# Performance work log

Measured on AMD Instinct MI355X. Metric: run time of the kernel, lower is better.

## Reference

```python
import jax, jax.numpy as jnp
import numpy as np
import math

B, S, HID = 2, 2048, 1024
NH = 16
HD = HID // NH


def setup_inputs() -> dict:
    key = jax.random.key(0)
    ks = jax.random.split(key, 5)
    std = 1.0 / math.sqrt(HID)
    return {
        "x": jax.random.normal(ks[0], (B, S, HID), dtype=jnp.float32),
        "wq": jax.random.normal(ks[1], (HID, HID), dtype=jnp.float32) * std,
        "wk": jax.random.normal(ks[2], (HID, HID), dtype=jnp.float32) * std,
        "wv": jax.random.normal(ks[3], (HID, HID), dtype=jnp.float32) * std,
        "wo": jax.random.normal(ks[4], (HID, HID), dtype=jnp.float32) * std,
    }


def reference(x, wq, wk, wv, wo):
    # x: [B, S, HID]; weights stored as nn.Linear weight [out, in] -> y = x @ W.T
    b, s, _ = x.shape
    scale = 1.0 / math.sqrt(HD)

    def heads(t):  # [B, S, HID] -> [B, NH, S, HD]
        return t.reshape(b, s, NH, HD).transpose(0, 2, 1, 3)

    q = heads(x @ wq.T)
    k = heads(x @ wk.T)
    v = heads(x @ wv.T)

    # single ring step (cp_size=1): streaming-LSE causal attention
    scores = jnp.einsum("bhqd,bhkd->bhqk", q, k) * scale  # [B, NH, S, S]
    q_idx = jnp.arange(s)[:, None]
    k_idx = jnp.arange(s)[None, :]
    causal_mask = k_idx > q_idx  # [S, S]
    scores = jnp.where(causal_mask, -jnp.inf, scores)

    local_max = jnp.max(scores, axis=-1, keepdims=True)
    exp_scores = jnp.exp(scores - local_max)
    local_sum = jnp.sum(exp_scores, axis=-1, keepdims=True)
    attn_num = jnp.einsum("bhqk,bhkd->bhqd", exp_scores, v)
    attn_out = attn_num / (local_sum + 1e-8)  # [B, NH, S, HD]

    attn_out = attn_out.transpose(0, 2, 1, 3).reshape(b, s, HID)
    return attn_out @ wo.T
```

## Files before the change

kernel.cpp:

```cpp
#include <hip/hip_runtime.h>
#include <hip/hip_bf16.h>

#define S_LEN 2048
#define NHEAD 16
#define HDIM 64
#define HID 1024
#define BATCH 2
#define TSTR 136

typedef __attribute__((ext_vector_type(8))) short s16x8;
typedef __attribute__((ext_vector_type(4))) short s16x4;
typedef __attribute__((ext_vector_type(4))) float f32x4;

__device__ __forceinline__ short f2bf(float f) {
    union { __hip_bfloat16 b; short s; } u;
    u.b = __float2bfloat16(f);
    return u.s;
}
__device__ __forceinline__ float fexp2(float x) {
    return __builtin_amdgcn_exp2f(x);
}
__device__ __forceinline__ f32x4 mfma16(s16x8 a, s16x8 b, f32x4 c) {
    return __builtin_amdgcn_mfma_f32_16x16x32_bf16(a, b, c, 0, 0, 0);
}
__device__ __forceinline__ void gload16(const short* g, short* l) {
    __builtin_amdgcn_global_load_lds(
        (const __attribute__((address_space(1))) void*)g,
        (__attribute__((address_space(3))) void*)l, 16, 0, 0);
}
__device__ __forceinline__ unsigned bfpack(float a, float b) {
    unsigned ua = __builtin_bit_cast(unsigned, a) + 0x8000u;
    unsigned ub = __builtin_bit_cast(unsigned, b) + 0x8000u;
    return (ub & 0xFFFF0000u) | (ua >> 16);
}

__global__ __launch_bounds__(256) void convert_kernel(
    const float* __restrict__ x,  const float* __restrict__ wq,
    const float* __restrict__ wk, const float* __restrict__ wv,
    const float* __restrict__ wo,
    short* __restrict__ xb, short* __restrict__ wcat, short* __restrict__ wob)
{
    const int F4X = 1048576, F4W = 262144;
    const int total = F4X + 4 * F4W;
    for (int i = blockIdx.x * blockDim.x + threadIdx.x; i < total;
         i += gridDim.x * blockDim.x) {
        const float4* s; short* d; int off;
        if (i < F4X)              { s = (const float4*)x;  d = xb;             off = i; }
        else if (i < F4X + F4W)   { s = (const float4*)wq; d = wcat;           off = i - F4X; }
        else if (i < F4X + 2*F4W) { s = (const float4*)wk; d = wcat + 1048576; off = i - (F4X + F4W); }
        else if (i < F4X + 3*F4W) { s = (const float4*)wv; d = wcat + 2097152; off = i - (F4X + 2*F4W); }
        else                      { s = (const float4*)wo; d = wob;            off = i - (F4X + 3*F4W); }
        float4 v = s[off];
        s16x4 o4 = { f2bf(v.x), f2bf(v.y), f2bf(v.z), f2bf(v.w) };
        *(s16x4*)(d + (size_t)off * 4) = o4;
    }
}

__global__ __launch_bounds__(256) void qkv_gemm2(
    const short* __restrict__ xb, const short* __restrict__ wcat,
    short* __restrict__ q_ws, short* __restrict__ k_ws, short* __restrict__ vt_ws)
{
    __shared__ union SM {
        struct { short A[128][64]; short B[128][64]; } s;
        short T[128][TSTR];
    } sm;
    const int t = threadIdx.x;
    const int lane = t & 63, w = t >> 6;
    const int g = lane >> 4, r15 = lane & 15;
    const int wm = w >> 1, wn = w & 1;
    const int bid = blockIdx.x;
    const int cx = bid & 7, ii = bid >> 3;
    const int mt = cx * 4 + (ii & 3), nt = ii >> 2;
    const int m0 = mt * 128, n0 = nt * 128;
    const int sel = n0 >> 10;
    const int nr0 = n0 & 1023;
    const short* Ag = (sel == 2) ? (wcat + (size_t)(2048 + nr0) * 1024)
                                 : (xb   + (size_t)m0 * 1024);
    const short* Bg = (sel == 2) ? (xb   + (size_t)m0 * 1024)
                                 : (wcat + (size_t)(sel * 1024 + nr0) * 1024);
    const int lrow = lane >> 3;
    const int scol = ((lane & 7) ^ lrow) * 8;
    const int rsw = r15 & 7;

    f32x4 acc[4][4] = {};

    for (int k0 = 0; k0 < 1024; k0 += 64) {
        __syncthreads();
        #pragma unroll
        for (int ch = 0; ch < 4; ++ch) {
            const int row = w * 32 + ch * 8;
            gload16(Ag + (size_t)(row + lrow) * 1024 + k0 + scol, &sm.s.A[row][0]);
            gload16(Bg + (size_t)(row + lrow) * 1024 + k0 + scol, &sm.s.B[row][0]);
        }
        __syncthreads();
        #pragma unroll
        for (int kk = 0; kk < 2; ++kk) {
            s16x8 af[4], bfr[4];
            #pragma unroll
            for (int mi = 0; mi < 4; ++mi)
                af[mi] = *(const s16x8*)&sm.s.A[wm * 64 + mi * 16 + r15][((kk * 4 + g) ^ rsw) * 8];
            #pragma unroll
            for (int ni = 0; ni < 4; ++ni)
                bfr[ni] = *(const s16x8*)&sm.s.B[wn * 64 + ni * 16 + r15][((kk * 4 + g) ^ rsw) * 8];
            #pragma unroll
            for (int mi = 0; mi < 4; ++mi)
                #pragma unroll
                for (int ni = 0; ni < 4; ++ni)
                    acc[mi][ni] = mfma16(af[mi], bfr[ni], acc[mi][ni]);
        }
    }

    __syncthreads();
    #pragma unroll
    for (int mi = 0; mi < 4; ++mi)
    #pragma unroll
    for (int ni = 0; ni < 4; ++ni)
        #pragma unroll
        for (int reg = 0; reg < 4; ++reg)
            sm.T[wm * 64 + mi * 16 + g * 4 + reg][wn * 64 + ni * 16 + r15]
                = f2bf(acc[mi][ni][reg]);
    __syncthreads();

    const int b = m0 >> 11;
    const int ms = m0 & 2047;
    #pragma unroll
    for (int it = 0; it < 8; ++it) {
        int u = w + it * 4;
        int half = u & 1;
        int rg = u >> 1;
        int r = rg * 8 + lrow;
        int colc = half * 64 + (lane & 7) * 8;
        s16x8 v = *(const s16x8*)&sm.T[r][colc];
        if (sel == 2) {
            int n = nr0 + r;
            int h = n >> 6, d = n & 63;
            *(s16x8*)(vt_ws + ((size_t)(b * NHEAD + h) * HDIM + d) * S_LEN + ms + colc) = v;
        } else {
            int s = ms + r;
            int n = nr0 + colc;
            int h = n >> 6, d = n & 63;
            short* dst = (sel == 0) ? q_ws : k_ws;
            *(s16x8*)(dst + ((size_t)(b * NHEAD + h) * S_LEN + s) * HDIM + d) = v;
        }
    }
}

__global__ __launch_bounds__(256) void attn_kernel2(
    const short* __restrict__ q_ws, const short* __restrict__ k_ws,
    const short* __restrict__ vt_ws, short* __restrict__ attn_ws)
{
    __shared__ short Ks[2][64][64];
    __shared__ short Vts[2][64][64];
    const int t = threadIdx.x;
    const int lane = t & 63, w = t >> 6;
    const int g = lane >> 4, r15 = lane & 15;
    const int bid = blockIdx.x;
    const int lb = (bid & 7) * 64 + (bid >> 3);
    const int p = lb & 15;
    const int bh = lb >> 4;
    const size_t base = (size_t)bh * S_LEN * HDIM;
    const float KSC = 0.18033688f;
    const int swr = (r15 & 7) << 3;
    const int r0 = t >> 3, c0 = (t & 7) * 8;
    const int cx0 = c0 ^ ((r0 & 7) << 3);
    const int b = bh >> 4, h = bh & 15;
    const int qloc = w * 16 + r15;

    union P8 { unsigned u[4]; s16x8 v; };
    union V8 { s16x4 h[2]; s16x8 v; };

    for (int phase = 0; phase < 2; ++phase) {
        const int qt = phase ? (31 - p) : p;
        const int q0 = qt * 64;
        const int ntk = qt + 1;
        const int qg = q0 + qloc;
        s16x8 qf0 = *(const s16x8*)(q_ws + base + (size_t)qg * HDIM + g * 8);
        s16x8 qf1 = *(const s16x8*)(q_ws + base + (size_t)qg * HDIM + 32 + g * 8);
        f32x4 o[4] = {};
        float mrun = -1e30f, lrun_p = 0.f;

        *(s16x8*)&Ks[0][r0][cx0]        = *(const s16x8*)(k_ws  + base + (size_t)r0 * HDIM + c0);
        *(s16x8*)&Ks[0][r0 + 32][cx0]   = *(const s16x8*)(k_ws  + base + (size_t)(r0 + 32) * HDIM + c0);
        *(s16x8*)&Vts[0][r0][cx0]       = *(const s16x8*)(vt_ws + base + (size_t)r0 * S_LEN + c0);
        *(s16x8*)&Vts[0][r0 + 32][cx0]  = *(const s16x8*)(vt_ws + base + (size_t)(r0 + 32) * S_LEN + c0);
        __syncthreads();

        const short* kpa = k_ws  + base + (size_t)(64 + r0) * HDIM + c0;
        const short* kpb = kpa + 32 * HDIM;
        const short* vpa = vt_ws + base + (size_t)r0 * S_LEN + 64 + c0;
        const short* vpb = vpa + 32 * S_LEN;

        for (int kt = 0; kt < ntk; ++kt) {
            const int cur = kt & 1;
            const bool pre = (kt + 1 < ntk);
            const bool dg = (kt == ntk - 1);
            s16x8 ka, kb, va, vb;
            if (pre) {
                ka = *(const s16x8*)kpa;  kb = *(const s16x8*)kpb;
                va = *(const s16x8*)vpa;  vb = *(const s16x8*)vpb;
                kpa += 64 * HDIM; kpb += 64 * HDIM; vpa += 64; vpb += 64;
            }

            s16x8 kfa[4][2];
            #pragma unroll
            for (int f = 0; f < 4; ++f)
                #pragma unroll
                for (int c = 0; c < 2; ++c)
                    kfa[f][c] = *(const s16x8*)&Ks[cur][f * 16 + r15][(c * 32 + g * 8) ^ swr];
            V8 vfr[4][2];
            #pragma unroll
            for (int f2 = 0; f2 < 4; ++f2)
                #pragma unroll
                for (int kc = 0; kc < 2; ++kc) {
                    vfr[f2][kc].h[0] = *(const s16x4*)&Vts[cur][f2 * 16 + r15][(kc * 32 + g * 4) ^ swr];
                    vfr[f2][kc].h[1] = *(const s16x4*)&Vts[cur][f2 * 16 + r15][(kc * 32 + 16 + g * 4) ^ swr];
                }

            f32x4 z[4];
            __builtin_amdgcn_s_setprio(1);
            #pragma unroll
            for (int f = 0; f < 4; ++f) {
                f32x4 zz = { 0.f, 0.f, 0.f, 0.f };
                zz = mfma16(kfa[f][0], qf0, zz);
                zz = mfma16(kfa[f][1], qf1, zz);
                z[f] = zz;
            }
            __builtin_amdgcn_s_setprio(0);

            if (dg) {
                #pragma unroll
                for (int f = 0; f < 4; ++f)
                    #pragma unroll
                    for (int reg = 0; reg < 4; ++reg)
                        if (f * 16 + g * 4 + reg > qloc) z[f][reg] = -3e30f;
            }

            float zf[4];
            #pragma unroll
            for (int f = 0; f < 4; ++f)
                zf[f] = fmaxf(fmaxf(z[f][0], z[f][1]), fmaxf(z[f][2], z[f][3]));
            float zm = fmaxf(fmaxf(zf[0], zf[1]), fmaxf(zf[2], zf[3]));
            zm = fmaxf(zm, __shfl_xor(zm, 16));
            zm = fmaxf(zm, __shfl_xor(zm, 32));
            float pm = zm * KSC;

            if (!__all(pm - mrun <= 8.0f)) {
                float newm = fmaxf(mrun, pm);
                float sc = fexp2(mrun - newm);
                #pragma unroll
                for (int f2 = 0; f2 < 4; ++f2) o[f2] *= sc;
                lrun_p *= sc;
                mrun = newm;
            }

            P8 p8[2];
            #pragma unroll
            for (int f = 0; f < 4; ++f) {
                float e0 = fexp2(__builtin_fmaf(z[f][0], KSC, -mrun));
                float e1 = fexp2(__builtin_fmaf(z[f][1], KSC, -mrun));
                float e2 = fexp2(__builtin_fmaf(z[f][2], KSC, -mrun));
                float e3 = fexp2(__builtin_fmaf(z[f][3], KSC, -mrun));
                lrun_p += (e0 + e1) + (e2 + e3);
                p8[f >> 1].u[(f & 1) * 2]     = bfpack(e0, e1);
                p8[f >> 1].u[(f & 1) * 2 + 1] = bfpack(e2, e3);
            }

            __builtin_amdgcn_s_setprio(1);
            #pragma unroll
            for (int f2 = 0; f2 < 4; ++f2) {
                o[f2] = mfma16(vfr[f2][0].v, p8[0].v, o[f2]);
                o[f2] = mfma16(vfr[f2][1].v, p8[1].v, o[f2]);
            }
            __builtin_amdgcn_s_setprio(0);

            if (pre) {
                *(s16x8*)&Ks[cur ^ 1][r0][cx0]       = ka;
                *(s16x8*)&Ks[cur ^ 1][r0 + 32][cx0]  = kb;
                *(s16x8*)&Vts[cur ^ 1][r0][cx0]      = va;
                *(s16x8*)&Vts[cur ^ 1][r0 + 32][cx0] = vb;
            }
            __syncthreads();
        }

        float lr = lrun_p;
        lr += __shfl_xor(lr, 16);
        lr += __shfl_xor(lr, 32);
        float inv = 1.f / (lr + 1e-8f);
        size_t obase = ((size_t)b * S_LEN + qg) * HID + h * HDIM + g * 4;
        #pragma unroll
        for (int f2 = 0; f2 < 4; ++f2) {
            s16x4 ov = { f2bf(o[f2][0] * inv), f2bf(o[f2][1] * inv),
                         f2bf(o[f2][2] * inv), f2bf(o[f2][3] * inv) };
            *(s16x4*)(attn_ws + obase + f2 * 16) = ov;
        }
    }
}

__global__ __launch_bounds__(256) void wo_gemm2(
    const short* __restrict__ attn, const short* __restrict__ wob,
    float* __restrict__ out)
{
    __shared__ short As[128][64];
    __shared__ short Bs[128][64];
    const int t = threadIdx.x;
    const int lane = t & 63, w = t >> 6;
    const int g = lane >> 4, r15 = lane & 15;
    const int wm = w >> 1, wn = w & 1;
    const int bid = blockIdx.x;
    const int cx = bid & 7, ii = bid >> 3;
    const int mt = cx * 4 + (ii & 3), nt = ii >> 2;
    const int m0 = mt * 128, n0 = nt * 128;
    const int lrow = lane >> 3;
    const int scol = ((lane & 7) ^ lrow) * 8;
    const int rsw = r15 & 7;

    f32x4 acc[4][4] = {};

    for (int k0 = 0; k0 < 1024; k0 += 64) {
        __syncthreads();
        #pragma unroll
        for (int ch = 0; ch < 4; ++ch) {
            const int row = w * 32 + ch * 8;
            gload16(attn + (size_t)(m0 + row + lrow) * 1024 + k0 + scol, &As[row][0]);
            gload16(wob  + (size_t)(n0 + row + lrow) * 1024 + k0 + scol, &Bs[row][0]);
        }
        __syncthreads();
        #pragma unroll
        for (int kk = 0; kk < 2; ++kk) {
            s16x8 af[4], bfr[4];
            #pragma unroll
            for (int mi = 0; mi < 4; ++mi)
                af[mi] = *(const s16x8*)&As[wm * 64 + mi * 16 + r15][((kk * 4 + g) ^ rsw) * 8];
            #pragma unroll
            for (int ni = 0; ni < 4; ++ni)
                bfr[ni] = *(const s16x8*)&Bs[wn * 64 + ni * 16 + r15][((kk * 4 + g) ^ rsw) * 8];
            #pragma unroll
            for (int mi = 0; mi < 4; ++mi)
                #pragma unroll
                for (int ni = 0; ni < 4; ++ni)
                    acc[mi][ni] = mfma16(af[mi], bfr[ni], acc[mi][ni]);
        }
    }

    #pragma unroll
    for (int mi = 0; mi < 4; ++mi)
    #pragma unroll
    for (int ni = 0; ni < 4; ++ni) {
        #pragma unroll
        for (int reg = 0; reg < 4; ++reg) {
            int m = m0 + wm * 64 + mi * 16 + g * 4 + reg;
            int n = n0 + wn * 64 + ni * 16 + r15;
            out[(size_t)m * 1024 + n] = acc[mi][ni][reg];
        }
    }
}

extern "C" void kernel_launch(void* const* d_in, const int* in_sizes, int n_in,
                              void* d_out, int out_size, void* d_ws, size_t ws_size,
                              hipStream_t stream) {
    const float* x  = (const float*)d_in[0];
    const float* wq = (const float*)d_in[1];
    const float* wk = (const float*)d_in[2];
    const float* wv = (const float*)d_in[3];
    const float* wo = (const float*)d_in[4];
    float* out = (float*)d_out;

    const size_t ELEMS = (size_t)BATCH * S_LEN * HID;
    short* q_ws    = (short*)d_ws;
    short* k_ws    = q_ws + ELEMS;
    short* vt_ws   = k_ws + ELEMS;
    short* xb      = vt_ws + ELEMS;
    short* attn_ws = xb;
    short* wcat    = xb + ELEMS;
    short* wob     = wcat + 3145728;

    convert_kernel<<<dim3(2048), dim3(256), 0, stream>>>(x, wq, wk, wv, wo, xb, wcat, wob);
    qkv_gemm2<<<dim3(768), dim3(256), 0, stream>>>(xb, wcat, q_ws, k_ws, vt_ws);
    attn_kernel2<<<dim3(512), dim3(256), 0, stream>>>(q_ws, k_ws, vt_ws, attn_ws);
    wo_gemm2<<<dim3(256), dim3(256), 0, stream>>>(attn_ws, wob, out);
}
```

Measured before the change: 120.4 us.

## Use direct global-to-LDS K/V loads and one heaviest-first q-tile per block

```diff
diff --git a/kernel.cpp b/kernel.cpp
--- a/kernel.cpp
+++ b/kernel.cpp
@@ -145,7 +145,7 @@
     }
 }
 
-__global__ __launch_bounds__(256) void attn_kernel2(
+__global__ __launch_bounds__(256) void attn_kernel3(
     const short* __restrict__ q_ws, const short* __restrict__ k_ws,
     const short* __restrict__ vt_ws, short* __restrict__ attn_ws)
 {
@@ -155,144 +155,136 @@
     const int lane = t & 63, w = t >> 6;
     const int g = lane >> 4, r15 = lane & 15;
     const int bid = blockIdx.x;
-    const int lb = (bid & 7) * 64 + (bid >> 3);
-    const int p = lb & 15;
-    const int bh = lb >> 4;
+    const int lb = (bid & 7) * 128 + (bid >> 3);
+    const int qt = 31 - (lb & 31);
+    const int bh = lb >> 5;
     const size_t base = (size_t)bh * S_LEN * HDIM;
     const float KSC = 0.18033688f;
     const int swr = (r15 & 7) << 3;
-    const int r0 = t >> 3, c0 = (t & 7) * 8;
-    const int cx0 = c0 ^ ((r0 & 7) << 3);
     const int b = bh >> 4, h = bh & 15;
     const int qloc = w * 16 + r15;
 
+    const int srow = w * 16 + (lane >> 3);
+    const int csrc = ((lane & 7) ^ ((lane >> 3) & 7)) * 8;
+
     union P8 { unsigned u[4]; s16x8 v; };
     union V8 { s16x4 h[2]; s16x8 v; };
 
-    for (int phase = 0; phase < 2; ++phase) {
-        const int qt = phase ? (31 - p) : p;
-        const int q0 = qt * 64;
-        const int ntk = qt + 1;
-        const int qg = q0 + qloc;
-        s16x8 qf0 = *(const s16x8*)(q_ws + base + (size_t)qg * HDIM + g * 8);
-        s16x8 qf1 = *(const s16x8*)(q_ws + base + (size_t)qg * HDIM + 32 + g * 8);
-        f32x4 o[4] = {};
-        float mrun = -1e30f, lrun_p = 0.f;
-
-        *(s16x8*)&Ks[0][r0][cx0]        = *(const s16x8*)(k_ws  + base + (size_t)r0 * HDIM + c0);
-        *(s16x8*)&Ks[0][r0 + 32][cx0]   = *(const s16x8*)(k_ws  + base + (size_t)(r0 + 32) * HDIM + c0);
-        *(s16x8*)&Vts[0][r0][cx0]       = *(const s16x8*)(vt_ws + base + (size_t)r0 * S_LEN + c0);
-        *(s16x8*)&Vts[0][r0 + 32][cx0]  = *(const s16x8*)(vt_ws + base + (size_t)(r0 + 32) * S_LEN + c0);
-        __syncthreads();
-
-        const short* kpa = k_ws  + base + (size_t)(64 + r0) * HDIM + c0;
-        const short* kpb = kpa + 32 * HDIM;
-        const short* vpa = vt_ws + base + (size_t)r0 * S_LEN + 64 + c0;
-        const short* vpb = vpa + 32 * S_LEN;
-
-        for (int kt = 0; kt < ntk; ++kt) {
-            const int cur = kt & 1;
-            const bool pre = (kt + 1 < ntk);
-            const bool dg = (kt == ntk - 1);
-            s16x8 ka, kb, va, vb;
-            if (pre) {
-                ka = *(const s16x8*)kpa;  kb = *(const s16x8*)kpb;
-                va = *(const s16x8*)vpa;  vb = *(const s16x8*)vpb;
-                kpa += 64 * HDIM; kpb += 64 * HDIM; vpa += 64; vpb += 64;
+    const int q0 = qt * 64;
+    const int ntk = qt + 1;
+    const int qg = q0 + qloc;
+    s16x8 qf0 = *(const s16x8*)(q_ws + base + (size_t)qg * HDIM + g * 8);
+    s16x8 qf1 = *(const s16x8*)(q_ws + base + (size_t)qg * HDIM + 32 + g * 8);
+    f32x4 o[4] = {};
+    float mrun = -1e30f, lrun_p = 0.f;
+
+    const short* kp = k_ws  + base + (size_t)srow * HDIM + csrc;
+    const short* vp = vt_ws + base + (size_t)srow * S_LEN + csrc;
+
+    gload16(kp,               &Ks[0][w * 16][0]);
+    gload16(kp + 8 * HDIM,    &Ks[0][w * 16 + 8][0]);
+    gload16(vp,               &Vts[0][w * 16][0]);
+    gload16(vp + 8 * S_LEN,   &Vts[0][w * 16 + 8][0]);
+    kp += 64 * HDIM; vp += 64;
+    __syncthreads();
+
+    for (int kt = 0; kt < ntk; ++kt) {
+        const int cur = kt & 1;
+        const bool dg = (kt == ntk - 1);
+
+        if (kt + 1 < ntk) {
+            gload16(kp,             &Ks[cur ^ 1][w * 16][0]);
+            gload16(kp + 8 * HDIM,  &Ks[cur ^ 1][w * 16 + 8][0]);
+            gload16(vp,             &Vts[cur ^ 1][w * 16][0]);
+            gload16(vp + 8 * S_LEN, &Vts[cur ^ 1][w * 16 + 8][0]);
+            kp += 64 * HDIM; vp += 64;
+        }
+
+        s16x8 kfa[4][2];
+        #pragma unroll
+        for (int f = 0; f < 4; ++f)
+            #pragma unroll
+            for (int c = 0; c < 2; ++c)
+                kfa[f][c] = *(const s16x8*)&Ks[cur][f * 16 + r15][(c * 32 + g * 8) ^ swr];
+        V8 vfr[4][2];
+        #pragma unroll
+        for (int f2 = 0; f2 < 4; ++f2)
+            #pragma unroll
+            for (int kc = 0; kc < 2; ++kc) {
+                vfr[f2][kc].h[0] = *(const s16x4*)&Vts[cur][f2 * 16 + r15][(kc * 32 + g * 4) ^ swr];
+                vfr[f2][kc].h[1] = *(const s16x4*)&Vts[cur][f2 * 16 + r15][(kc * 32 + 16 + g * 4) ^ swr];
             }
 
-            s16x8 kfa[4][2];
+        f32x4 z[4];
+        __builtin_amdgcn_s_setprio(1);
+        #pragma unroll
+        for (int f = 0; f < 4; ++f) {
+            f32x4 zz = { 0.f, 0.f, 0.f, 0.f };
+            zz = mfma16(kfa[f][0], qf0, zz);
+            zz = mfma16(kfa[f][1], qf1, zz);
+            z[f] = zz;
+        }
+        __builtin_amdgcn_s_setprio(0);
+
+        if (dg) {
             #pragma unroll
             for (int f = 0; f < 4; ++f)
                 #pragma unroll
-                for (int c = 0; c < 2; ++c)
-                    kfa[f][c] = *(const s16x8*)&Ks[cur][f * 16 + r15][(c * 32 + g * 8) ^ swr];
-            V8 vfr[4][2];
-            #pragma unroll
-            for (int f2 = 0; f2 < 4; ++f2)
-                #pragma unroll
-                for (int kc = 0; kc < 2; ++kc) {
-                    vfr[f2][kc].h[0] = *(const s16x4*)&Vts[cur][f2 * 16 + r15][(kc * 32 + g * 4) ^ swr];
-                    vfr[f2][kc].h[1] = *(const s16x4*)&Vts[cur][f2 * 16 + r15][(kc * 32 + 16 + g * 4) ^ swr];
-                }
-
-            f32x4 z[4];
-            __builtin_amdgcn_s_setprio(1);
-            #pragma unroll
-            for (int f = 0; f < 4; ++f) {
-                f32x4 zz = { 0.f, 0.f, 0.f, 0.f };
-                zz = mfma16(kfa[f][0], qf0, zz);
-                zz = mfma16(kfa[f][1], qf1, zz);
-                z[f] = zz;
-            }
-            __builtin_amdgcn_s_setprio(0);
-
-            if (dg) {
-                #pragma unroll
-                for (int f = 0; f < 4; ++f)
-                    #pragma unroll
-                    for (int reg = 0; reg < 4; ++reg)
-                        if (f * 16 + g * 4 + reg > qloc) z[f][reg] = -3e30f;
-            }
-
-            float zf[4];
-            #pragma unroll
-            for (int f = 0; f < 4; ++f)
-                zf[f] = fmaxf(fmaxf(z[f][0], z[f][1]), fmaxf(z[f][2], z[f][3]));
-            float zm = fmaxf(fmaxf(zf[0], zf[1]), fmaxf(zf[2], zf[3]));
-            zm = fmaxf(zm, __shfl_xor(zm, 16));
-            zm = fmaxf(zm, __shfl_xor(zm, 32));
-            float pm = zm * KSC;
-
-            if (!__all(pm - mrun <= 8.0f)) {
-                float newm = fmaxf(mrun, pm);
-                float sc = fexp2(mrun - newm);
-                #pragma unroll
-                for (int f2 = 0; f2 < 4; ++f2) o[f2] *= sc;
-                lrun_p *= sc;
-                mrun = newm;
-            }
-
-            P8 p8[2];
-            #pragma unroll
-            for (int f = 0; f < 4; ++f) {
-                float e0 = fexp2(__builtin_fmaf(z[f][0], KSC, -mrun));
-                float e1 = fexp2(__builtin_fmaf(z[f][1], KSC, -mrun));
-                float e2 = fexp2(__builtin_fmaf(z[f][2], KSC, -mrun));
-                float e3 = fexp2(__builtin_fmaf(z[f][3], KSC, -mrun));
-                lrun_p += (e0 + e1) + (e2 + e3);
-                p8[f >> 1].u[(f & 1) * 2]     = bfpack(e0, e1);
-                p8[f >> 1].u[(f & 1) * 2 + 1] = bfpack(e2, e3);
-            }
-
-            __builtin_amdgcn_s_setprio(1);
-            #pragma unroll
-            for (int f2 = 0; f2 < 4; ++f2) {
-                o[f2] = mfma16(vfr[f2][0].v, p8[0].v, o[f2]);
-                o[f2] = mfma16(vfr[f2][1].v, p8[1].v, o[f2]);
-            }
-            __builtin_amdgcn_s_setprio(0);
-
-            if (pre) {
-                *(s16x8*)&Ks[cur ^ 1][r0][cx0]       = ka;
-                *(s16x8*)&Ks[cur ^ 1][r0 + 32][cx0]  = kb;
-                *(s16x8*)&Vts[cur ^ 1][r0][cx0]      = va;
-                *(s16x8*)&Vts[cur ^ 1][r0 + 32][cx0] = vb;
-            }
-            __syncthreads();
-        }
-
-        float lr = lrun_p;
-        lr += __shfl_xor(lr, 16);
-        lr += __shfl_xor(lr, 32);
-        float inv = 1.f / (lr + 1e-8f);
-        size_t obase = ((size_t)b * S_LEN + qg) * HID + h * HDIM + g * 4;
+                for (int reg = 0; reg < 4; ++reg)
+                    if (f * 16 + g * 4 + reg > qloc) z[f][reg] = -3e30f;
+        }
+
+        float zf[4];
+        #pragma unroll
+        for (int f = 0; f < 4; ++f)
+            zf[f] = fmaxf(fmaxf(z[f][0], z[f][1]), fmaxf(z[f][2], z[f][3]));
+        float zm = fmaxf(fmaxf(zf[0], zf[1]), fmaxf(zf[2], zf[3]));
+        zm = fmaxf(zm, __shfl_xor(zm, 16));
+        zm = fmaxf(zm, __shfl_xor(zm, 32));
+        float pm = zm * KSC;
+
+        if (!__all(pm - mrun <= 8.0f)) {
+            float newm = fmaxf(mrun, pm);
+            float sc = fexp2(mrun - newm);
+            #pragma unroll
+            for (int f2 = 0; f2 < 4; ++f2) o[f2] *= sc;
+            lrun_p *= sc;
+            mrun = newm;
+        }
+
+        P8 p8[2];
+        #pragma unroll
+        for (int f = 0; f < 4; ++f) {
+            float e0 = fexp2(__builtin_fmaf(z[f][0], KSC, -mrun));
+            float e1 = fexp2(__builtin_fmaf(z[f][1], KSC, -mrun));
+            float e2 = fexp2(__builtin_fmaf(z[f][2], KSC, -mrun));
+            float e3 = fexp2(__builtin_fmaf(z[f][3], KSC, -mrun));
+            lrun_p += (e0 + e1) + (e2 + e3);
+            p8[f >> 1].u[(f & 1) * 2]     = bfpack(e0, e1);
+            p8[f >> 1].u[(f & 1) * 2 + 1] = bfpack(e2, e3);
+        }
+
+        __builtin_amdgcn_s_setprio(1);
         #pragma unroll
         for (int f2 = 0; f2 < 4; ++f2) {
-            s16x4 ov = { f2bf(o[f2][0] * inv), f2bf(o[f2][1] * inv),
-                         f2bf(o[f2][2] * inv), f2bf(o[f2][3] * inv) };
-            *(s16x4*)(attn_ws + obase + f2 * 16) = ov;
-        }
+            o[f2] = mfma16(vfr[f2][0].v, p8[0].v, o[f2]);
+            o[f2] = mfma16(vfr[f2][1].v, p8[1].v, o[f2]);
+        }
+        __builtin_amdgcn_s_setprio(0);
+
+        __syncthreads();
+    }
+
+    float lr = lrun_p;
+    lr += __shfl_xor(lr, 16);
+    lr += __shfl_xor(lr, 32);
+    float inv = 1.f / (lr + 1e-8f);
+    size_t obase = ((size_t)b * S_LEN + qg) * HID + h * HDIM + g * 4;
+    #pragma unroll
+    for (int f2 = 0; f2 < 4; ++f2) {
+        s16x4 ov = { f2bf(o[f2][0] * inv), f2bf(o[f2][1] * inv),
+                     f2bf(o[f2][2] * inv), f2bf(o[f2][3] * inv) };
+        *(s16x4*)(attn_ws + obase + f2 * 16) = ov;
     }
 }
 
@@ -376,6 +368,6 @@
 
     convert_kernel<<<dim3(2048), dim3(256), 0, stream>>>(x, wq, wk, wv, wo, xb, wcat, wob);
     qkv_gemm2<<<dim3(768), dim3(256), 0, stream>>>(xb, wcat, q_ws, k_ws, vt_ws);
-    attn_kernel2<<<dim3(512), dim3(256), 0, stream>>>(q_ws, k_ws, vt_ws, attn_ws);
+    attn_kernel3<<<dim3(1024), dim3(256), 0, stream>>>(q_ws, k_ws, vt_ws, attn_ws);
     wo_gemm2<<<dim3(256), dim3(256), 0, stream>>>(attn_ws, wob, out);
 }
```

Measured after the change: 144.7 us. +20.2%, slower.

## Widen attention tile to 256 queries per block with 8 waves sharing K/V

Applied to the files above, without the earlier changes.

```diff
diff --git a/kernel.cpp b/kernel.cpp
--- a/kernel.cpp
+++ b/kernel.cpp
@@ -145,7 +145,7 @@
     }
 }
 
-__global__ __launch_bounds__(256) void attn_kernel2(
+__global__ __launch_bounds__(512) void attn_kernel4(
     const short* __restrict__ q_ws, const short* __restrict__ k_ws,
     const short* __restrict__ vt_ws, short* __restrict__ attn_ws)
 {
@@ -155,51 +155,54 @@
     const int lane = t & 63, w = t >> 6;
     const int g = lane >> 4, r15 = lane & 15;
     const int bid = blockIdx.x;
-    const int lb = (bid & 7) * 64 + (bid >> 3);
-    const int p = lb & 15;
-    const int bh = lb >> 4;
+    const int lb = (bid & 7) * 32 + (bid >> 3);
+    const int bh = lb >> 3;
+    const int qi = lb & 7;
     const size_t base = (size_t)bh * S_LEN * HDIM;
     const float KSC = 0.18033688f;
     const int swr = (r15 & 7) << 3;
+    const int b = bh >> 4, h = bh & 15;
+
+    const int q0 = qi * 256;
+    const int ntk = 4 * qi + 4;
+    const int ktlast = 4 * qi + (w >> 1);
+    const int qrel = (w & 1) * 32 + r15;
+
     const int r0 = t >> 3, c0 = (t & 7) * 8;
     const int cx0 = c0 ^ ((r0 & 7) << 3);
-    const int b = bh >> 4, h = bh & 15;
-    const int qloc = w * 16 + r15;
 
     union P8 { unsigned u[4]; s16x8 v; };
     union V8 { s16x4 h[2]; s16x8 v; };
 
-    for (int phase = 0; phase < 2; ++phase) {
-        const int qt = phase ? (31 - p) : p;
-        const int q0 = qt * 64;
-        const int ntk = qt + 1;
-        const int qg = q0 + qloc;
-        s16x8 qf0 = *(const s16x8*)(q_ws + base + (size_t)qg * HDIM + g * 8);
-        s16x8 qf1 = *(const s16x8*)(q_ws + base + (size_t)qg * HDIM + 32 + g * 8);
-        f32x4 o[4] = {};
-        float mrun = -1e30f, lrun_p = 0.f;
-
-        *(s16x8*)&Ks[0][r0][cx0]        = *(const s16x8*)(k_ws  + base + (size_t)r0 * HDIM + c0);
-        *(s16x8*)&Ks[0][r0 + 32][cx0]   = *(const s16x8*)(k_ws  + base + (size_t)(r0 + 32) * HDIM + c0);
-        *(s16x8*)&Vts[0][r0][cx0]       = *(const s16x8*)(vt_ws + base + (size_t)r0 * S_LEN + c0);
-        *(s16x8*)&Vts[0][r0 + 32][cx0]  = *(const s16x8*)(vt_ws + base + (size_t)(r0 + 32) * S_LEN + c0);
-        __syncthreads();
-
-        const short* kpa = k_ws  + base + (size_t)(64 + r0) * HDIM + c0;
-        const short* kpb = kpa + 32 * HDIM;
-        const short* vpa = vt_ws + base + (size_t)r0 * S_LEN + 64 + c0;
-        const short* vpb = vpa + 32 * S_LEN;
-
-        for (int kt = 0; kt < ntk; ++kt) {
-            const int cur = kt & 1;
-            const bool pre = (kt + 1 < ntk);
-            const bool dg = (kt == ntk - 1);
-            s16x8 ka, kb, va, vb;
-            if (pre) {
-                ka = *(const s16x8*)kpa;  kb = *(const s16x8*)kpb;
-                va = *(const s16x8*)vpa;  vb = *(const s16x8*)vpb;
-                kpa += 64 * HDIM; kpb += 64 * HDIM; vpa += 64; vpb += 64;
-            }
+    s16x8 qf[2][2];
+    #pragma unroll
+    for (int m = 0; m < 2; ++m)
+        #pragma unroll
+        for (int c = 0; c < 2; ++c)
+            qf[m][c] = *(const s16x8*)(q_ws + base +
+                (size_t)(q0 + w * 32 + m * 16 + r15) * HDIM + c * 32 + g * 8);
+
+    f32x4 o[2][4] = {};
+    float mrun[2] = { -1e30f, -1e30f }, lrun[2] = { 0.f, 0.f };
+
+    *(s16x8*)&Ks[0][r0][cx0]  = *(const s16x8*)(k_ws  + base + (size_t)r0 * HDIM + c0);
+    *(s16x8*)&Vts[0][r0][cx0] = *(const s16x8*)(vt_ws + base + (size_t)r0 * S_LEN + c0);
+    __syncthreads();
+
+    const short* kp = k_ws  + base + (size_t)(64 + r0) * HDIM + c0;
+    const short* vp = vt_ws + base + (size_t)r0 * S_LEN + 64 + c0;
+
+    for (int kt = 0; kt < ntk; ++kt) {
+        const int cur = kt & 1;
+        const bool pre = (kt + 1 < ntk);
+        s16x8 ka, va;
+        if (pre) {
+            ka = *(const s16x8*)kp;  va = *(const s16x8*)vp;
+            kp += 64 * HDIM; vp += 64;
+        }
+
+        if (kt <= ktlast) {
+            const bool dg = (kt == ktlast);
 
             s16x8 kfa[4][2];
             #pragma unroll
@@ -216,81 +219,87 @@
                     vfr[f2][kc].h[1] = *(const s16x4*)&Vts[cur][f2 * 16 + r15][(kc * 32 + 16 + g * 4) ^ swr];
                 }
 
-            f32x4 z[4];
-            __builtin_amdgcn_s_setprio(1);
-            #pragma unroll
-            for (int f = 0; f < 4; ++f) {
-                f32x4 zz = { 0.f, 0.f, 0.f, 0.f };
-                zz = mfma16(kfa[f][0], qf0, zz);
-                zz = mfma16(kfa[f][1], qf1, zz);
-                z[f] = zz;
+            #pragma unroll
+            for (int m = 0; m < 2; ++m) {
+                f32x4 z[4];
+                __builtin_amdgcn_s_setprio(1);
+                #pragma unroll
+                for (int f = 0; f < 4; ++f) {
+                    f32x4 zz = { 0.f, 0.f, 0.f, 0.f };
+                    zz = mfma16(kfa[f][0], qf[m][0], zz);
+                    zz = mfma16(kfa[f][1], qf[m][1], zz);
+                    z[f] = zz;
+                }
+                __builtin_amdgcn_s_setprio(0);
+
+                if (dg) {
+                    const int qr = qrel + m * 16;
+                    #pragma unroll
+                    for (int f = 0; f < 4; ++f)
+                        #pragma unroll
+                        for (int reg = 0; reg < 4; ++reg)
+                            if (f * 16 + g * 4 + reg > qr) z[f][reg] = -3e30f;
+                }
+
+                float zf[4];
+                #pragma unroll
+                for (int f = 0; f < 4; ++f)
+                    zf[f] = fmaxf(fmaxf(z[f][0], z[f][1]), fmaxf(z[f][2], z[f][3]));
+                float zm = fmaxf(fmaxf(zf[0], zf[1]), fmaxf(zf[2], zf[3]));
+                zm = fmaxf(zm, __shfl_xor(zm, 16));
+                zm = fmaxf(zm, __shfl_xor(zm, 32));
+                float pm = zm * KSC;
+
+                if (!__all(pm - mrun[m] <= 8.0f)) {
+                    float newm = fmaxf(mrun[m], pm);
+                    float sc = fexp2(mrun[m] - newm);
+                    #pragma unroll
+                    for (int f2 = 0; f2 < 4; ++f2) o[m][f2] *= sc;
+                    lrun[m] *= sc;
+                    mrun[m] = newm;
+                }
+
+                P8 p8[2];
+                #pragma unroll
+                for (int f = 0; f < 4; ++f) {
+                    float e0 = fexp2(__builtin_fmaf(z[f][0], KSC, -mrun[m]));
+                    float e1 = fexp2(__builtin_fmaf(z[f][1], KSC, -mrun[m]));
+                    float e2 = fexp2(__builtin_fmaf(z[f][2], KSC, -mrun[m]));
+                    float e3 = fexp2(__builtin_fmaf(z[f][3], KSC, -mrun[m]));
+                    lrun[m] += (e0 + e1) + (e2 + e3);
+                    p8[f >> 1].u[(f & 1) * 2]     = bfpack(e0, e1);
+                    p8[f >> 1].u[(f & 1) * 2 + 1] = bfpack(e2, e3);
+                }
+
+                __builtin_amdgcn_s_setprio(1);
+                #pragma unroll
+                for (int f2 = 0; f2 < 4; ++f2) {
+                    o[m][f2] = mfma16(vfr[f2][0].v, p8[0].v, o[m][f2]);
+                    o[m][f2] = mfma16(vfr[f2][1].v, p8[1].v, o[m][f2]);
+                }
+                __builtin_amdgcn_s_setprio(0);
             }
-            __builtin_amdgcn_s_setprio(0);
-
-            if (dg) {
-                #pragma unroll
-                for (int f = 0; f < 4; ++f)
-                    #pragma unroll
-                    for (int reg = 0; reg < 4; ++reg)
-                        if (f * 16 + g * 4 + reg > qloc) z[f][reg] = -3e30f;
-            }
-
-            float zf[4];
-            #pragma unroll
-            for (int f = 0; f < 4; ++f)
-                zf[f] = fmaxf(fmaxf(z[f][0], z[f][1]), fmaxf(z[f][2], z[f][3]));
-            float zm = fmaxf(fmaxf(zf[0], zf[1]), fmaxf(zf[2], zf[3]));
-            zm = fmaxf(zm, __shfl_xor(zm, 16));
-            zm = fmaxf(zm, __shfl_xor(zm, 32));
-            float pm = zm * KSC;
-
-            if (!__all(pm - mrun <= 8.0f)) {
-                float newm = fmaxf(mrun, pm);
-                float sc = fexp2(mrun - newm);
-                #pragma unroll
-                for (int f2 = 0; f2 < 4; ++f2) o[f2] *= sc;
-                lrun_p *= sc;
-                mrun = newm;
-            }
-
-            P8 p8[2];
-            #pragma unroll
-            for (int f = 0; f < 4; ++f) {
-                float e0 = fexp2(__builtin_fmaf(z[f][0], KSC, -mrun));
-                float e1 = fexp2(__builtin_fmaf(z[f][1], KSC, -mrun));
-                float e2 = fexp2(__builtin_fmaf(z[f][2], KSC, -mrun));
-                float e3 = fexp2(__builtin_fmaf(z[f][3], KSC, -mrun));
-                lrun_p += (e0 + e1) + (e2 + e3);
-                p8[f >> 1].u[(f & 1) * 2]     = bfpack(e0, e1);
-                p8[f >> 1].u[(f & 1) * 2 + 1] = bfpack(e2, e3);
-            }
-
-            __builtin_amdgcn_s_setprio(1);
-            #pragma unroll
-            for (int f2 = 0; f2 < 4; ++f2) {
-                o[f2] = mfma16(vfr[f2][0].v, p8[0].v, o[f2]);
-                o[f2] = mfma16(vfr[f2][1].v, p8[1].v, o[f2]);
-            }
-            __builtin_amdgcn_s_setprio(0);
-
-            if (pre) {
-                *(s16x8*)&Ks[cur ^ 1][r0][cx0]       = ka;
-                *(s16x8*)&Ks[cur ^ 1][r0 + 32][cx0]  = kb;
-                *(s16x8*)&Vts[cur ^ 1][r0][cx0]      = va;
-                *(s16x8*)&Vts[cur ^ 1][r0 + 32][cx0] = vb;
-            }
-            __syncthreads();
-        }
-
-        float lr = lrun_p;
+        }
+
+        if (pre) {
+            *(s16x8*)&Ks[cur ^ 1][r0][cx0]  = ka;
+            *(s16x8*)&Vts[cur ^ 1][r0][cx0] = va;
+        }
+        __syncthreads();
+    }
+
+    #pragma unroll
+    for (int m = 0; m < 2; ++m) {
+        float lr = lrun[m];
         lr += __shfl_xor(lr, 16);
         lr += __shfl_xor(lr, 32);
         float inv = 1.f / (lr + 1e-8f);
+        const int qg = q0 + w * 32 + m * 16 + r15;
         size_t obase = ((size_t)b * S_LEN + qg) * HID + h * HDIM + g * 4;
         #pragma unroll
         for (int f2 = 0; f2 < 4; ++f2) {
-            s16x4 ov = { f2bf(o[f2][0] * inv), f2bf(o[f2][1] * inv),
-                         f2bf(o[f2][2] * inv), f2bf(o[f2][3] * inv) };
+            s16x4 ov = { f2bf(o[m][f2][0] * inv), f2bf(o[m][f2][1] * inv),
+                         f2bf(o[m][f2][2] * inv), f2bf(o[m][f2][3] * inv) };
             *(s16x4*)(attn_ws + obase + f2 * 16) = ov;
         }
     }
@@ -376,6 +385,6 @@
 
     convert_kernel<<<dim3(2048), dim3(256), 0, stream>>>(x, wq, wk, wv, wo, xb, wcat, wob);
     qkv_gemm2<<<dim3(768), dim3(256), 0, stream>>>(xb, wcat, q_ws, k_ws, vt_ws);
-    attn_kernel2<<<dim3(512), dim3(256), 0, stream>>>(q_ws, k_ws, vt_ws, attn_ws);
+    attn_kernel4<<<dim3(256), dim3(512), 0, stream>>>(q_ws, k_ws, vt_ws, attn_ws);
     wo_gemm2<<<dim3(256), dim3(256), 0, stream>>>(attn_ws, wob, out);
 }
```

Measured after the change: 140.8 us. 16.9% more time.

## Split attention into 32-row query tiles with 128-thread blocks

Applied to the files above, without the earlier changes.

```diff
diff --git a/kernel.cpp b/kernel.cpp
--- a/kernel.cpp
+++ b/kernel.cpp
@@ -145,7 +145,7 @@
     }
 }
 
-__global__ __launch_bounds__(256) void attn_kernel2(
+__global__ __launch_bounds__(128) void attn_kernel5(
     const short* __restrict__ q_ws, const short* __restrict__ k_ws,
     const short* __restrict__ vt_ws, short* __restrict__ attn_ws)
 {
@@ -155,50 +155,54 @@
     const int lane = t & 63, w = t >> 6;
     const int g = lane >> 4, r15 = lane & 15;
     const int bid = blockIdx.x;
-    const int lb = (bid & 7) * 64 + (bid >> 3);
-    const int p = lb & 15;
-    const int bh = lb >> 4;
+    const int lb = (bid & 7) * 128 + (bid >> 3);
+    const int pi = lb & 31;
+    const int bh = lb >> 5;
     const size_t base = (size_t)bh * S_LEN * HDIM;
     const float KSC = 0.18033688f;
     const int swr = (r15 & 7) << 3;
+    const int b = bh >> 4, h = bh & 15;
+
     const int r0 = t >> 3, c0 = (t & 7) * 8;
     const int cx0 = c0 ^ ((r0 & 7) << 3);
-    const int b = bh >> 4, h = bh & 15;
-    const int qloc = w * 16 + r15;
 
     union P8 { unsigned u[4]; s16x8 v; };
     union V8 { s16x4 h[2]; s16x8 v; };
 
     for (int phase = 0; phase < 2; ++phase) {
-        const int qt = phase ? (31 - p) : p;
-        const int q0 = qt * 64;
-        const int ntk = qt + 1;
-        const int qg = q0 + qloc;
+        const int qt32 = phase ? (63 - pi) : pi;
+        const int q0 = qt32 * 32;
+        const int ntk = (qt32 >> 1) + 1;
+        const int qg = q0 + w * 16 + r15;
+        const int qrel = qg - (ntk - 1) * 64;
         s16x8 qf0 = *(const s16x8*)(q_ws + base + (size_t)qg * HDIM + g * 8);
         s16x8 qf1 = *(const s16x8*)(q_ws + base + (size_t)qg * HDIM + 32 + g * 8);
         f32x4 o[4] = {};
         float mrun = -1e30f, lrun_p = 0.f;
 
-        *(s16x8*)&Ks[0][r0][cx0]        = *(const s16x8*)(k_ws  + base + (size_t)r0 * HDIM + c0);
-        *(s16x8*)&Ks[0][r0 + 32][cx0]   = *(const s16x8*)(k_ws  + base + (size_t)(r0 + 32) * HDIM + c0);
-        *(s16x8*)&Vts[0][r0][cx0]       = *(const s16x8*)(vt_ws + base + (size_t)r0 * S_LEN + c0);
-        *(s16x8*)&Vts[0][r0 + 32][cx0]  = *(const s16x8*)(vt_ws + base + (size_t)(r0 + 32) * S_LEN + c0);
-        __syncthreads();
-
-        const short* kpa = k_ws  + base + (size_t)(64 + r0) * HDIM + c0;
-        const short* kpb = kpa + 32 * HDIM;
-        const short* vpa = vt_ws + base + (size_t)r0 * S_LEN + 64 + c0;
-        const short* vpb = vpa + 32 * S_LEN;
+        #pragma unroll
+        for (int j = 0; j < 4; ++j) {
+            int r = r0 + j * 16;
+            *(s16x8*)&Ks[0][r][cx0]  = *(const s16x8*)(k_ws  + base + (size_t)r * HDIM + c0);
+            *(s16x8*)&Vts[0][r][cx0] = *(const s16x8*)(vt_ws + base + (size_t)r * S_LEN + c0);
+        }
+        __syncthreads();
+
+        const short* kp = k_ws  + base + (size_t)(64 + r0) * HDIM + c0;
+        const short* vp = vt_ws + base + (size_t)r0 * S_LEN + 64 + c0;
 
         for (int kt = 0; kt < ntk; ++kt) {
             const int cur = kt & 1;
             const bool pre = (kt + 1 < ntk);
             const bool dg = (kt == ntk - 1);
-            s16x8 ka, kb, va, vb;
+            s16x8 ka[4], va[4];
             if (pre) {
-                ka = *(const s16x8*)kpa;  kb = *(const s16x8*)kpb;
-                va = *(const s16x8*)vpa;  vb = *(const s16x8*)vpb;
-                kpa += 64 * HDIM; kpb += 64 * HDIM; vpa += 64; vpb += 64;
+                #pragma unroll
+                for (int j = 0; j < 4; ++j) {
+                    ka[j] = *(const s16x8*)(kp + (size_t)j * 16 * HDIM);
+                    va[j] = *(const s16x8*)(vp + (size_t)j * 16 * S_LEN);
+                }
+                kp += (size_t)64 * HDIM; vp += 64;
             }
 
             s16x8 kfa[4][2];
@@ -232,7 +236,7 @@
                 for (int f = 0; f < 4; ++f)
                     #pragma unroll
                     for (int reg = 0; reg < 4; ++reg)
-                        if (f * 16 + g * 4 + reg > qloc) z[f][reg] = -3e30f;
+                        if (f * 16 + g * 4 + reg > qrel) z[f][reg] = -3e30f;
             }
 
             float zf[4];
@@ -274,10 +278,12 @@
             __builtin_amdgcn_s_setprio(0);
 
             if (pre) {
-                *(s16x8*)&Ks[cur ^ 1][r0][cx0]       = ka;
-                *(s16x8*)&Ks[cur ^ 1][r0 + 32][cx0]  = kb;
-                *(s16x8*)&Vts[cur ^ 1][r0][cx0]      = va;
-                *(s16x8*)&Vts[cur ^ 1][r0 + 32][cx0] = vb;
+                #pragma unroll
+                for (int j = 0; j < 4; ++j) {
+                    int r = r0 + j * 16;
+                    *(s16x8*)&Ks[cur ^ 1][r][cx0]  = ka[j];
+                    *(s16x8*)&Vts[cur ^ 1][r][cx0] = va[j];
+                }
             }
             __syncthreads();
         }
@@ -293,6 +299,7 @@
                          f2bf(o[f2][2] * inv), f2bf(o[f2][3] * inv) };
             *(s16x4*)(attn_ws + obase + f2 * 16) = ov;
         }
+        __syncthreads();
     }
 }
 
@@ -376,6 +383,6 @@
 
     convert_kernel<<<dim3(2048), dim3(256), 0, stream>>>(x, wq, wk, wv, wo, xb, wcat, wob);
     qkv_gemm2<<<dim3(768), dim3(256), 0, stream>>>(xb, wcat, q_ws, k_ws, vt_ws);
-    attn_kernel2<<<dim3(512), dim3(256), 0, stream>>>(q_ws, k_ws, vt_ws, attn_ws);
+    attn_kernel5<<<dim3(1024), dim3(128), 0, stream>>>(q_ws, k_ws, vt_ws, attn_ws);
     wo_gemm2<<<dim3(256), dim3(256), 0, stream>>>(attn_ws, wob, out);
 }
```

After: 123.3 us. 1.02x slower.
